# Optimization experiments

Measured on AMD Instinct MI355X. Metric: run time of the kernel, lower is better.

Reference implementation:

```python
import jax, jax.numpy as jnp
import numpy as np

N_NODES = 50000
N_EDGES = 800000
D_IN = 512
D_OUT = 256

def setup_inputs() -> dict:
    key = jax.random.key(0)
    k1, k2, k3, k4, k5 = jax.random.split(key, 5)
    return {
        "inputs": jax.random.normal(k1, (N_NODES, D_IN), dtype=jnp.float32),
        "weights": jax.random.uniform(k2, (D_IN, D_OUT), dtype=jnp.float32, minval=-0.1, maxval=0.1),
        "bias": jnp.zeros((D_OUT,), dtype=jnp.float32),
        "edge_vals": jax.random.uniform(k3, (N_EDGES,), dtype=jnp.float32),
        "edge_row": jax.random.randint(k4, (N_EDGES,), 0, N_NODES),
        "edge_col": jax.random.randint(k5, (N_EDGES,), 0, N_NODES),
    }

def reference(inputs, weights, bias, edge_vals, edge_row, edge_col):
    # dense projection: [N, D_in] @ [D_in, D_out] -> [N, D_out]
    supports = inputs @ weights
    # sparse adjacency spmm in COO form: out[i] = sum_e vals[e] * supports[col[e]] for row[e] == i
    msgs = supports[edge_col] * edge_vals[:, None]  # [E, D_out]
    aggregated = jax.ops.segment_sum(msgs, edge_row, num_segments=inputs.shape[0])
    return aggregated + bias
```

## Files before the change

kernel.cpp:

```cpp
#include <hip/hip_runtime.h>

#define D_IN 512
#define D_OUT 256
#define BM 64
#define BK 32
#define LDK 40

typedef short short8 __attribute__((ext_vector_type(8)));
typedef float floatx4 __attribute__((ext_vector_type(4)));

static __device__ __forceinline__ unsigned short f2bf(float f) {
    unsigned u = __float_as_uint(f);
    u += 0x7FFF + ((u >> 16) & 1);
    return (unsigned short)(u >> 16);
}
static __device__ __forceinline__ float bf2f(unsigned short h) {
    return __uint_as_float((unsigned)h << 16);
}

#define CONV_BLOCKS 256
__global__ __launch_bounds__(512) void convert_and_zero(const float* __restrict__ W,
                                                        unsigned short* __restrict__ Wt,
                                                        int* __restrict__ cnt, int M) {
    int b = blockIdx.x;
    if (b < CONV_BLOCKS) {
        int t = b * 512 + threadIdx.x;
        int n = t >> 9;
        int k = t & 511;
        Wt[t] = f2bf(W[(size_t)k * D_OUT + n]);
    } else {
        int i = (b - CONV_BLOCKS) * 512 + threadIdx.x;
        if (i < M) cnt[i] = 0;
    }
}

__global__ __launch_bounds__(256) void hist_rows(const int* __restrict__ rows,
                                                 int* __restrict__ cnt, int E) {
    int e = blockIdx.x * 256 + threadIdx.x;
    if (e < E) atomicAdd(&cnt[rows[e]], 1);
}

#define SCAN_B 4096
__global__ __launch_bounds__(1024) void scan_blocks(const int* __restrict__ cnt,
                                                    int* __restrict__ ptr,
                                                    int* __restrict__ partials, int M) {
    __shared__ int wsum[16];
    const int t = threadIdx.x, lane = t & 63, wave = t >> 6;
    const int base = blockIdx.x * SCAN_B + t * 4;
    int4 v = make_int4(0, 0, 0, 0);
    if (base + 3 < M) v = *(const int4*)(cnt + base);
    else {
        if (base + 0 < M) v.x = cnt[base + 0];
        if (base + 1 < M) v.y = cnt[base + 1];
        if (base + 2 < M) v.z = cnt[base + 2];
        if (base + 3 < M) v.w = cnt[base + 3];
    }
    int s = v.x + v.y + v.z + v.w;
    int incl = s;
#pragma unroll
    for (int off = 1; off < 64; off <<= 1) {
        int x = __shfl_up(incl, off, 64);
        if (lane >= off) incl += x;
    }
    if (lane == 63) wsum[wave] = incl;
    __syncthreads();
    if (t == 0) {
        int run = 0;
#pragma unroll
        for (int w = 0; w < 16; ++w) { int x = wsum[w]; wsum[w] = run; run += x; }
        partials[blockIdx.x] = run;
    }
    __syncthreads();
    int e0 = wsum[wave] + (incl - s);
    int e1 = e0 + v.x, e2 = e1 + v.y, e3 = e2 + v.z;
    if (base + 3 < M) *(int4*)(ptr + base) = make_int4(e0, e1, e2, e3);
    else {
        if (base + 0 < M) ptr[base + 0] = e0;
        if (base + 1 < M) ptr[base + 1] = e1;
        if (base + 2 < M) ptr[base + 2] = e2;
        if (base + 3 < M) ptr[base + 3] = e3;
    }
}

__global__ __launch_bounds__(64) void scan_partials(int* __restrict__ partials,
                                                    int* __restrict__ ptr, int M, int nb) {
    const int t = threadIdx.x;
    int v = (t < nb) ? partials[t] : 0;
    int incl = v;
#pragma unroll
    for (int off = 1; off < 64; off <<= 1) {
        int x = __shfl_up(incl, off, 64);
        if (t >= off) incl += x;
    }
    if (t < nb) partials[t] = incl - v;
    if (t == 63) ptr[M] = incl;
}

__global__ __launch_bounds__(256) void add_offsets(int* __restrict__ ptr,
                                                   const int* __restrict__ partials,
                                                   int M) {
    int i = blockIdx.x * 256 + threadIdx.x;
    if (i < M) ptr[i] += partials[i >> 12];
}

__global__ __launch_bounds__(512, 4) void gemm_build(
    const float* __restrict__ A, const unsigned short* __restrict__ Wt,
    unsigned short* __restrict__ S, int M, int nGemm,
    const float* __restrict__ vals, const int* __restrict__ rows,
    const int* __restrict__ cols, int* __restrict__ ptr,
    int2* __restrict__ edges, int E) {
    __shared__ unsigned short As[BM * LDK];
    __shared__ unsigned short Bs[D_OUT * LDK];
    const int tid = threadIdx.x;

    if ((int)blockIdx.x >= nGemm) {
        int e = ((int)blockIdx.x - nGemm) * 512 + tid;
        if (e < E) {
            int r = rows[e];
            int pos = atomicAdd(&ptr[r], 1);
            edges[pos] = make_int2(cols[e], __float_as_int(vals[e]));
        }
        return;
    }

    const int lane = tid & 63;
    const int wave = tid >> 6;
    const int wn   = wave * 32;
    const int bm   = blockIdx.x * BM;
    const int l15  = lane & 15;
    const int quad = lane >> 4;

    const int am   = tid >> 3;
    const int ak4  = (tid & 7) * 4;
    const bool aval = (bm + am) < M;
    const float* aptr = A + (size_t)(aval ? bm + am : 0) * D_IN + ak4;
    const int aoff = am * LDK + ak4;

    const unsigned short* bptr[2];
    int boff[2];
#pragma unroll
    for (int i = 0; i < 2; ++i) {
        int item = tid + i * 512;
        int bn = item >> 2;
        int k8 = (item & 3) * 8;
        bptr[i] = Wt + (size_t)bn * D_IN + k8;
        boff[i] = bn * LDK + k8;
    }

    float4 aR = aval ? *(const float4*)aptr : make_float4(0.f, 0.f, 0.f, 0.f);
    short8 bR[2];
#pragma unroll
    for (int i = 0; i < 2; ++i) bR[i] = *(const short8*)(bptr[i]);

    floatx4 acc[4][2] = {};

    for (int k0 = 0; k0 < D_IN; k0 += BK) {
        ushort4 ab;
        ab.x = f2bf(aR.x); ab.y = f2bf(aR.y); ab.z = f2bf(aR.z); ab.w = f2bf(aR.w);
        *(ushort4*)(As + aoff) = ab;
#pragma unroll
        for (int i = 0; i < 2; ++i) *(short8*)(Bs + boff[i]) = bR[i];
        __syncthreads();

        if (k0 + BK < D_IN) {
            aR = aval ? *(const float4*)(aptr + k0 + BK)
                      : make_float4(0.f, 0.f, 0.f, 0.f);
#pragma unroll
            for (int i = 0; i < 2; ++i) bR[i] = *(const short8*)(bptr[i] + k0 + BK);
        }

        short8 af[4], bfr[2];
#pragma unroll
        for (int i = 0; i < 4; ++i)
            af[i] = *(const short8*)(As + (i * 16 + l15) * LDK + quad * 8);
#pragma unroll
        for (int j = 0; j < 2; ++j)
            bfr[j] = *(const short8*)(Bs + (wn + j * 16 + l15) * LDK + quad * 8);
#pragma unroll
        for (int i = 0; i < 4; ++i)
#pragma unroll
            for (int j = 0; j < 2; ++j)
                acc[i][j] = __builtin_amdgcn_mfma_f32_16x16x32_bf16(
                    af[i], bfr[j], acc[i][j], 0, 0, 0);
        __syncthreads();
    }

#pragma unroll
    for (int i = 0; i < 4; ++i) {
#pragma unroll
        for (int r = 0; r < 4; ++r) {
            int gm = bm + i * 16 + quad * 4 + r;
            if (gm < M) {
#pragma unroll
                for (int j = 0; j < 2; ++j)
                    S[(size_t)gm * D_OUT + wn + j * 16 + l15] = f2bf(acc[i][j][r]);
            }
        }
    }
}

__global__ __launch_bounds__(256) void spmm_rows(const unsigned short* __restrict__ S,
                                                 const int2* __restrict__ edges,
                                                 const int* __restrict__ ptr,
                                                 const float* __restrict__ bias,
                                                 float* __restrict__ out, int M) {
    const int row = blockIdx.x * 4 + (threadIdx.x >> 6);
    if (row >= M) return;
    const int lane = threadIdx.x & 63;
    float4 a0 = ((const float4*)bias)[lane];
    float4 a1 = make_float4(0.f, 0.f, 0.f, 0.f);
    const int beg = row ? ptr[row - 1] : 0;
    const int end = ptr[row];
    int j = beg;
    for (; j + 7 < end; j += 8) {
        int2 e0 = edges[j + 0], e1 = edges[j + 1], e2 = edges[j + 2], e3 = edges[j + 3];
        int2 e4 = edges[j + 4], e5 = edges[j + 5], e6 = edges[j + 6], e7 = edges[j + 7];
        ushort4 s0 = ((const ushort4*)(S + (size_t)e0.x * D_OUT))[lane];
        ushort4 s1 = ((const ushort4*)(S + (size_t)e1.x * D_OUT))[lane];
        ushort4 s2 = ((const ushort4*)(S + (size_t)e2.x * D_OUT))[lane];
        ushort4 s3 = ((const ushort4*)(S + (size_t)e3.x * D_OUT))[lane];
        ushort4 s4 = ((const ushort4*)(S + (size_t)e4.x * D_OUT))[lane];
        ushort4 s5 = ((const ushort4*)(S + (size_t)e5.x * D_OUT))[lane];
        ushort4 s6 = ((const ushort4*)(S + (size_t)e6.x * D_OUT))[lane];
        ushort4 s7 = ((const ushort4*)(S + (size_t)e7.x * D_OUT))[lane];
        float v0 = __int_as_float(e0.y), v1 = __int_as_float(e1.y);
        float v2 = __int_as_float(e2.y), v3 = __int_as_float(e3.y);
        float v4 = __int_as_float(e4.y), v5 = __int_as_float(e5.y);
        float v6 = __int_as_float(e6.y), v7 = __int_as_float(e7.y);
        a0.x += v0 * bf2f(s0.x) + v2 * bf2f(s2.x) + v4 * bf2f(s4.x) + v6 * bf2f(s6.x);
        a0.y += v0 * bf2f(s0.y) + v2 * bf2f(s2.y) + v4 * bf2f(s4.y) + v6 * bf2f(s6.y);
        a0.z += v0 * bf2f(s0.z) + v2 * bf2f(s2.z) + v4 * bf2f(s4.z) + v6 * bf2f(s6.z);
        a0.w += v0 * bf2f(s0.w) + v2 * bf2f(s2.w) + v4 * bf2f(s4.w) + v6 * bf2f(s6.w);
        a1.x += v1 * bf2f(s1.x) + v3 * bf2f(s3.x) + v5 * bf2f(s5.x) + v7 * bf2f(s7.x);
        a1.y += v1 * bf2f(s1.y) + v3 * bf2f(s3.y) + v5 * bf2f(s5.y) + v7 * bf2f(s7.y);
        a1.z += v1 * bf2f(s1.z) + v3 * bf2f(s3.z) + v5 * bf2f(s5.z) + v7 * bf2f(s7.z);
        a1.w += v1 * bf2f(s1.w) + v3 * bf2f(s3.w) + v5 * bf2f(s5.w) + v7 * bf2f(s7.w);
    }
    for (; j + 3 < end; j += 4) {
        int2 e0 = edges[j], e1 = edges[j + 1], e2 = edges[j + 2], e3 = edges[j + 3];
        ushort4 s0 = ((const ushort4*)(S + (size_t)e0.x * D_OUT))[lane];
        ushort4 s1 = ((const ushort4*)(S + (size_t)e1.x * D_OUT))[lane];
        ushort4 s2 = ((const ushort4*)(S + (size_t)e2.x * D_OUT))[lane];
        ushort4 s3 = ((const ushort4*)(S + (size_t)e3.x * D_OUT))[lane];
        float v0 = __int_as_float(e0.y), v1 = __int_as_float(e1.y);
        float v2 = __int_as_float(e2.y), v3 = __int_as_float(e3.y);
        a0.x += v0 * bf2f(s0.x) + v2 * bf2f(s2.x);
        a0.y += v0 * bf2f(s0.y) + v2 * bf2f(s2.y);
        a0.z += v0 * bf2f(s0.z) + v2 * bf2f(s2.z);
        a0.w += v0 * bf2f(s0.w) + v2 * bf2f(s2.w);
        a1.x += v1 * bf2f(s1.x) + v3 * bf2f(s3.x);
        a1.y += v1 * bf2f(s1.y) + v3 * bf2f(s3.y);
        a1.z += v1 * bf2f(s1.z) + v3 * bf2f(s3.z);
        a1.w += v1 * bf2f(s1.w) + v3 * bf2f(s3.w);
    }
    for (; j < end; ++j) {
        int2 e = edges[j];
        float v = __int_as_float(e.y);
        ushort4 s = ((const ushort4*)(S + (size_t)e.x * D_OUT))[lane];
        a0.x += v * bf2f(s.x);
        a0.y += v * bf2f(s.y);
        a0.z += v * bf2f(s.z);
        a0.w += v * bf2f(s.w);
    }
    a0.x += a1.x; a0.y += a1.y; a0.z += a1.z; a0.w += a1.w;
    floatx4 res = {a0.x, a0.y, a0.z, a0.w};
    __builtin_nontemporal_store(res, (floatx4*)(out + (size_t)row * D_OUT) + lane);
}

extern "C" void kernel_launch(void* const* d_in, const int* in_sizes, int n_in,
                              void* d_out, int out_size, void* d_ws, size_t ws_size,
                              hipStream_t stream) {
    const float* inputs    = (const float*)d_in[0];
    const float* weights   = (const float*)d_in[1];
    const float* bias      = (const float*)d_in[2];
    const float* edge_vals = (const float*)d_in[3];
    const int*   edge_row  = (const int*)d_in[4];
    const int*   edge_col  = (const int*)d_in[5];
    float* out = (float*)d_out;

    const int M = in_sizes[0] / D_IN;
    const int E = in_sizes[3];

    char* ws = (char*)d_ws;
    unsigned short* S  = (unsigned short*)ws;
    unsigned short* Wt = (unsigned short*)(ws + (size_t)M * D_OUT * 2);
    int2* edges        = (int2*)((char*)Wt + (size_t)D_OUT * D_IN * 2);
    int*  ptr          = (int*)((char*)edges + (size_t)E * 8);
    int*  cnt          = ptr + ((M + 4) & ~3);
    int*  partials     = cnt + M;

    int nzero = (M + 511) / 512;
    convert_and_zero<<<CONV_BLOCKS + nzero, 512, 0, stream>>>(weights, Wt, cnt, M);

    hist_rows<<<(E + 255) / 256, 256, 0, stream>>>(edge_row, cnt, E);
    int nb = (M + SCAN_B - 1) / SCAN_B;
    scan_blocks<<<nb, 1024, 0, stream>>>(cnt, ptr, partials, M);
    scan_partials<<<1, 64, 0, stream>>>(partials, ptr, M, nb);
    add_offsets<<<(M + 255) / 256, 256, 0, stream>>>(ptr, partials, M);

    int nGemm  = (M + BM - 1) / BM;
    int nBuild = (E + 511) / 512;
    gemm_build<<<nGemm + nBuild, 512, 0, stream>>>(inputs, Wt, S, M, nGemm,
                                                   edge_vals, edge_row, edge_col,
                                                   ptr, edges, E);

    spmm_rows<<<(M + 3) / 4, 256, 0, stream>>>(S, edges, ptr, bias, out, M);
}
```

Measured before the change: 311.1 us.

## Retile GEMM to 128x128, interleave edge-build blocks, and drop scan_partials kernel

The GEMM moves from 64-row tiles covering all 256 output columns to 128x128 tiles. Shared memory switches to a k-major, 8-wide layout without padding, and each thread now loads 8 floats of A and one 8-element B vector. Edge-scatter blocks are interleaved with GEMM blocks (every third block), so atomic-bound build work runs alongside MFMA work. Each build thread handles 4 edges with loads batched before the atomics and writes edges with nontemporal stores. The separate scan_partials launch is removed; add_offsets now sums the preceding block partials itself. This saves one launch but adds a small serial loop per thread, and ptr[M] is no longer written.

After: 332.5 us. 1.07x slower.

```diff
diff --git a/kernel.cpp b/kernel.cpp
--- a/kernel.cpp
+++ b/kernel.cpp
@@ -2,9 +2,9 @@
 
 #define D_IN 512
 #define D_OUT 256
-#define BM 64
+#define BM 128
+#define BN 128
 #define BK 32
-#define LDK 40
 
 typedef short short8 __attribute__((ext_vector_type(8)));
 typedef float floatx4 __attribute__((ext_vector_type(4)));
@@ -82,100 +82,101 @@
     }
 }
 
-__global__ __launch_bounds__(64) void scan_partials(int* __restrict__ partials,
-                                                    int* __restrict__ ptr, int M, int nb) {
-    const int t = threadIdx.x;
-    int v = (t < nb) ? partials[t] : 0;
-    int incl = v;
-#pragma unroll
-    for (int off = 1; off < 64; off <<= 1) {
-        int x = __shfl_up(incl, off, 64);
-        if (t >= off) incl += x;
-    }
-    if (t < nb) partials[t] = incl - v;
-    if (t == 63) ptr[M] = incl;
-}
-
 __global__ __launch_bounds__(256) void add_offsets(int* __restrict__ ptr,
                                                    const int* __restrict__ partials,
                                                    int M) {
     int i = blockIdx.x * 256 + threadIdx.x;
-    if (i < M) ptr[i] += partials[i >> 12];
+    if (i >= M) return;
+    int bucket = blockIdx.x >> 4;
+    int off = 0;
+    for (int j = 0; j < bucket; ++j) off += partials[j];
+    ptr[i] += off;
 }
 
 __global__ __launch_bounds__(512, 4) void gemm_build(
     const float* __restrict__ A, const unsigned short* __restrict__ Wt,
-    unsigned short* __restrict__ S, int M, int nGemm,
+    unsigned short* __restrict__ S, int M, int nGemm, int nBuild,
     const float* __restrict__ vals, const int* __restrict__ rows,
     const int* __restrict__ cols, int* __restrict__ ptr,
-    int2* __restrict__ edges, int E) {
-    __shared__ unsigned short As[BM * LDK];
-    __shared__ unsigned short Bs[D_OUT * LDK];
+    unsigned long long* __restrict__ edges, int E) {
+    __shared__ unsigned short As[4 * BM * 8];
+    __shared__ unsigned short Bs[4 * BN * 8];
+    const int bid = blockIdx.x;
     const int tid = threadIdx.x;
-
-    if ((int)blockIdx.x >= nGemm) {
-        int e = ((int)blockIdx.x - nGemm) * 512 + tid;
-        if (e < E) {
-            int r = rows[e];
-            int pos = atomicAdd(&ptr[r], 1);
-            edges[pos] = make_int2(cols[e], __float_as_int(vals[e]));
+    const int r3  = bid % 3;
+    const int p3  = bid / 3;
+
+    if (r3 == 2) {
+        if (p3 >= nBuild) return;
+        int e0 = p3 * 2048 + tid;
+        int rr[4]; unsigned cc[4], vv[4]; bool ok[4];
+#pragma unroll
+        for (int i = 0; i < 4; ++i) {
+            int e = e0 + i * 512;
+            ok[i] = e < E;
+            int es = ok[i] ? e : 0;
+            rr[i] = rows[es];
+            cc[i] = (unsigned)cols[es];
+            vv[i] = (unsigned)__float_as_int(vals[es]);
+        }
+#pragma unroll
+        for (int i = 0; i < 4; ++i) {
+            if (ok[i]) {
+                int pos = atomicAdd(&ptr[rr[i]], 1);
+                unsigned long long packed =
+                    (unsigned long long)cc[i] | ((unsigned long long)vv[i] << 32);
+                __builtin_nontemporal_store(packed, edges + pos);
+            }
         }
         return;
     }
 
+    const int gi = p3 * 2 + r3;
+    if (gi >= nGemm) return;
     const int lane = tid & 63;
     const int wave = tid >> 6;
-    const int wn   = wave * 32;
-    const int bm   = blockIdx.x * BM;
     const int l15  = lane & 15;
     const int quad = lane >> 4;
-
-    const int am   = tid >> 3;
-    const int ak4  = (tid & 7) * 4;
-    const bool aval = (bm + am) < M;
-    const float* aptr = A + (size_t)(aval ? bm + am : 0) * D_IN + ak4;
-    const int aoff = am * LDK + ak4;
-
-    const unsigned short* bptr[2];
-    int boff[2];
-#pragma unroll
-    for (int i = 0; i < 2; ++i) {
-        int item = tid + i * 512;
-        int bn = item >> 2;
-        int k8 = (item & 3) * 8;
-        bptr[i] = Wt + (size_t)bn * D_IN + k8;
-        boff[i] = bn * LDK + k8;
-    }
-
-    float4 aR = aval ? *(const float4*)aptr : make_float4(0.f, 0.f, 0.f, 0.f);
-    short8 bR[2];
-#pragma unroll
-    for (int i = 0; i < 2; ++i) bR[i] = *(const short8*)(bptr[i]);
+    const int bm   = (gi >> 1) * BM;
+    const int bn   = (gi & 1) * BN;
+    const int wm   = (wave >> 2) * 64;
+    const int wn   = (wave & 3) * 32;
+
+    const int sm = wave * 16 + l15;
+    const bool aval = (bm + sm) < M;
+    const float* aptr = A + (size_t)(aval ? bm + sm : 0) * D_IN + quad * 8;
+    const unsigned short* bptr = Wt + (size_t)(bn + sm) * D_IN + quad * 8;
+    const int soff = (quad * BM + sm) * 8;
+
+    float4 aR0 = aval ? *(const float4*)(aptr + 0) : make_float4(0.f, 0.f, 0.f, 0.f);
+    float4 aR1 = aval ? *(const float4*)(aptr + 4) : make_float4(0.f, 0.f, 0.f, 0.f);
+    short8 bR  = *(const short8*)bptr;
 
     floatx4 acc[4][2] = {};
 
     for (int k0 = 0; k0 < D_IN; k0 += BK) {
-        ushort4 ab;
-        ab.x = f2bf(aR.x); ab.y = f2bf(aR.y); ab.z = f2bf(aR.z); ab.w = f2bf(aR.w);
-        *(ushort4*)(As + aoff) = ab;
-#pragma unroll
-        for (int i = 0; i < 2; ++i) *(short8*)(Bs + boff[i]) = bR[i];
+        short8 a8;
+        a8[0] = (short)f2bf(aR0.x); a8[1] = (short)f2bf(aR0.y);
+        a8[2] = (short)f2bf(aR0.z); a8[3] = (short)f2bf(aR0.w);
+        a8[4] = (short)f2bf(aR1.x); a8[5] = (short)f2bf(aR1.y);
+        a8[6] = (short)f2bf(aR1.z); a8[7] = (short)f2bf(aR1.w);
+        *(short8*)(As + soff) = a8;
+        *(short8*)(Bs + soff) = bR;
         __syncthreads();
 
         if (k0 + BK < D_IN) {
-            aR = aval ? *(const float4*)(aptr + k0 + BK)
-                      : make_float4(0.f, 0.f, 0.f, 0.f);
-#pragma unroll
-            for (int i = 0; i < 2; ++i) bR[i] = *(const short8*)(bptr[i] + k0 + BK);
+            aR0 = aval ? *(const float4*)(aptr + k0 + BK + 0) : make_float4(0.f, 0.f, 0.f, 0.f);
+            aR1 = aval ? *(const float4*)(aptr + k0 + BK + 4) : make_float4(0.f, 0.f, 0.f, 0.f);
+            bR  = *(const short8*)(bptr + k0 + BK);
         }
 
         short8 af[4], bfr[2];
 #pragma unroll
         for (int i = 0; i < 4; ++i)
-            af[i] = *(const short8*)(As + (i * 16 + l15) * LDK + quad * 8);
+            af[i] = *(const short8*)(As + (quad * BM + wm + i * 16 + l15) * 8);
 #pragma unroll
         for (int j = 0; j < 2; ++j)
-            bfr[j] = *(const short8*)(Bs + (wn + j * 16 + l15) * LDK + quad * 8);
+            bfr[j] = *(const short8*)(Bs + (quad * BN + wn + j * 16 + l15) * 8);
 #pragma unroll
         for (int i = 0; i < 4; ++i)
 #pragma unroll
@@ -189,11 +190,11 @@
     for (int i = 0; i < 4; ++i) {
 #pragma unroll
         for (int r = 0; r < 4; ++r) {
-            int gm = bm + i * 16 + quad * 4 + r;
+            int gm = bm + wm + i * 16 + quad * 4 + r;
             if (gm < M) {
 #pragma unroll
                 for (int j = 0; j < 2; ++j)
-                    S[(size_t)gm * D_OUT + wn + j * 16 + l15] = f2bf(acc[i][j][r]);
+                    S[(size_t)gm * D_OUT + bn + wn + j * 16 + l15] = f2bf(acc[i][j][r]);
             }
         }
     }
@@ -284,7 +285,7 @@
     char* ws = (char*)d_ws;
     unsigned short* S  = (unsigned short*)ws;
     unsigned short* Wt = (unsigned short*)(ws + (size_t)M * D_OUT * 2);
-    int2* edges        = (int2*)((char*)Wt + (size_t)D_OUT * D_IN * 2);
+    unsigned long long* edges = (unsigned long long*)((char*)Wt + (size_t)D_OUT * D_IN * 2);
     int*  ptr          = (int*)((char*)edges + (size_t)E * 8);
     int*  cnt          = ptr + ((M + 4) & ~3);
     int*  partials     = cnt + M;
@@ -295,14 +296,14 @@
     hist_rows<<<(E + 255) / 256, 256, 0, stream>>>(edge_row, cnt, E);
     int nb = (M + SCAN_B - 1) / SCAN_B;
     scan_blocks<<<nb, 1024, 0, stream>>>(cnt, ptr, partials, M);
-    scan_partials<<<1, 64, 0, stream>>>(partials, ptr, M, nb);
     add_offsets<<<(M + 255) / 256, 256, 0, stream>>>(ptr, partials, M);
 
-    int nGemm  = (M + BM - 1) / BM;
-    int nBuild = (E + 511) / 512;
-    gemm_build<<<nGemm + nBuild, 512, 0, stream>>>(inputs, Wt, S, M, nGemm,
-                                                   edge_vals, edge_row, edge_col,
-                                                   ptr, edges, E);
-
-    spmm_rows<<<(M + 3) / 4, 256, 0, stream>>>(S, edges, ptr, bias, out, M);
-}
+    int nGemm  = 2 * ((M + BM - 1) / BM);
+    int nBuild = (E + 2047) / 2048;
+    int nPair  = nBuild > (nGemm + 1) / 2 ? nBuild : (nGemm + 1) / 2;
+    gemm_build<<<3 * nPair, 512, 0, stream>>>(inputs, Wt, S, M, nGemm, nBuild,
+                                              edge_vals, edge_row, edge_col,
+                                              ptr, edges, E);
+
+    spmm_rows<<<(M + 3) / 4, 256, 0, stream>>>(S, edges != 0 ? (const int2*)edges : (const int2*)edges, ptr, bias, out, M);
+}
```
